# Performance work log

Measured on AMD Instinct MI355X. Metric: run time of the kernel, lower is better.

## Reference

```python
import jax, jax.numpy as jnp
import numpy as np

N, D, E, T, R, KMEM, DE = 50000, 128, 800000, 400000, 1, 32, 16
EPS = 1e-5
BETA_MAX = 5.0
GRAD_CLIP = 1.0
STATE_CLIP = 10.0
STEP = 0.1
DAMP = 0.9999  # update_damping=1.0 clamped to 1-1e-4 as in __init__


def segment_logsumexp(s, idx, n):
    # numerically-stable per-segment logsumexp; empty segments contribute 0
    m = jax.ops.segment_max(s, idx, num_segments=n)
    ms = jnp.where(jnp.isfinite(m), m, 0.0)
    z = jax.ops.segment_sum(jnp.exp(s - ms[idx]), idx, num_segments=n)
    return jnp.where(z > 0, jnp.log(jnp.maximum(z, 1e-30)) + ms, 0.0)


def setup_inputs() -> dict:
    key = jax.random.key(0)
    ks = jax.random.split(key, 24)
    inv1 = jnp.log(jnp.expm1(jnp.float32(1.0)))  # _inv_softplus(1.0)
    xav = 0.5 * np.sqrt(2.0 / (2 * D))  # xavier_uniform gain=0.5 ~ std
    inp = {
        'X': jax.random.normal(ks[0], (N, D), jnp.float32),
        'edge_attr': jax.random.normal(ks[1], (E, DE), jnp.float32),
        'ln_gamma': jnp.ones((D,), jnp.float32),
        'ln_beta': jnp.zeros((D,), jnp.float32),
        'W_Q2': jax.random.normal(ks[2], (D, D), jnp.float32) * xav,
        'W_K2': jax.random.normal(ks[3], (D, D), jnp.float32) * xav,
        'W_Q3': jax.random.normal(ks[4], (D, R * D), jnp.float32) * xav,
        'W_K3': jax.random.normal(ks[5], (D, R * D), jnp.float32) * xav,
        'T_tau': jax.random.normal(ks[6], (2, R, D), jnp.float32) * 0.02,
        'W_Qm': jax.random.normal(ks[7], (D, D), jnp.float32) * xav,
        'W_Km': jax.random.normal(ks[8], (D, D), jnp.float32) * xav,
        'B_mem': jax.random.normal(ks[9], (KMEM, D), jnp.float32) / np.sqrt(D),
        'We1': jax.random.normal(ks[10], (DE, D), jnp.float32) / np.sqrt(DE),
        'be1': jnp.zeros((D,), jnp.float32),
        'We2': jax.random.normal(ks[11], (D, 1), jnp.float32) / np.sqrt(D),
        'be2': jnp.zeros((1,), jnp.float32),
        'lambda_2': inv1, 'lambda_3': inv1, 'lambda_m': inv1,
        'beta_2': inv1, 'beta_3': inv1, 'beta_m': inv1,
        'c_2': jax.random.randint(ks[12], (E,), 0, N),
        'u_2': jax.random.randint(ks[13], (E,), 0, N),
        'c_3': jax.random.randint(ks[14], (T,), 0, N),
        'u_3': jax.random.randint(ks[15], (T,), 0, N),
        'v_3': jax.random.randint(ks[16], (T,), 0, N),
        't_tau': jax.random.randint(ks[17], (T,), 0, 2),
    }
    return inp


def reference(X, edge_attr, ln_gamma, ln_beta, W_Q2, W_K2, W_Q3, W_K3, T_tau,
              W_Qm, W_Km, B_mem, We1, be1, We2, be2,
              lambda_2, lambda_3, lambda_m, beta_2, beta_3, beta_m,
              c_2, u_2, c_3, u_3, v_3, t_tau):
    sqrt_d = jnp.sqrt(jnp.float32(D))

    def energy(Xv):
        mu = jnp.mean(Xv, axis=-1, keepdims=True)
        var = jnp.var(Xv, axis=-1, keepdims=True)
        G = (Xv - mu) * jax.lax.rsqrt(var + EPS) * ln_gamma + ln_beta
        # pairwise (order-2) energy over edge list
        b2 = jnp.minimum(jax.nn.softplus(beta_2), BETA_MAX)
        Q2, K2 = G @ W_Q2, G @ W_K2
        a2 = (jax.nn.gelu(edge_attr @ We1 + be1) @ We2 + be2)[:, 0]  # edge_mlp bias
        s2 = b2 * (jnp.sum(Q2[c_2] * K2[u_2], axis=-1) / sqrt_d) + a2  # [E]
        E2 = -(jax.nn.softplus(lambda_2) / b2) * jnp.sum(segment_logsumexp(s2, c_2, N))
        # triplet (order-3) energy with per-type tensor T_tau
        b3 = jnp.minimum(jax.nn.softplus(beta_3), BETA_MAX)
        Q3 = (G @ W_Q3).reshape(-1, R, D)
        K3 = (G @ W_K3).reshape(-1, R, D)
        s3 = b3 * jnp.einsum('erd,erd,erd,erd->e', Q3[c_3], K3[u_3], K3[v_3],
                             T_tau[t_tau]) / jnp.float32(D)  # [T]
        E3 = -(jax.nn.softplus(lambda_3) / b3) * jnp.sum(segment_logsumexp(s3, c_3, N))
        # memory-bank energy
        bm = jnp.minimum(jax.nn.softplus(beta_m), BETA_MAX)
        sm = bm * ((G @ W_Qm) @ (B_mem @ W_Km).T) / sqrt_d  # [N,K]
        Em = -(jax.nn.softplus(lambda_m) / bm) * jnp.sum(jax.nn.logsumexp(sm, axis=1))
        return E2 + E3 + Em

    Eval, gX = jax.value_and_grad(energy)(X)
    gn = jnp.maximum(jnp.linalg.norm(gX, axis=-1, keepdims=True), 1e-6)
    gX = gX * jnp.minimum(GRAD_CLIP / gn, 1.0)
    X_next = X - STEP * DAMP * gX
    sn = jnp.maximum(jnp.linalg.norm(X_next, axis=-1, keepdims=True), 1e-6)
    X_next = X_next * jnp.minimum(STATE_CLIP / sn, 1.0)
    return (X_next, Eval)
```

## Files before the change

### kernel.cpp

```cpp
#include <hip/hip_runtime.h>

#define NN 50000
#define DD 128
#define EE 800000
#define TT 400000
#define KM 32
#define UU 320
#define ROWB 12500
#define MB 782
#define EDGE_BLKS 3125
#define HB2 391
#define HBT 196
#define WCB 320
#define ZCB 196
#define FWD_TOT 11532
#define SCAN_TILE 2048
#define SCAN_NB ((NN + SCAN_TILE - 1) / SCAN_TILE)

static constexpr float INV_SQRT_D = 0.08838834764831845f;
static constexpr float INV_D = 1.f / 128.f;

typedef __attribute__((ext_vector_type(8))) short bf16x8;
typedef __attribute__((ext_vector_type(4))) float f32x4;
typedef unsigned short ushort_t;

__device__ __forceinline__ float softplus_f(float x) {
  return (x > 20.f) ? x : log1pf(__expf(x));
}

__device__ __forceinline__ float gelu_fast(float x) {
  float p = fmaf(0.044715f * x * x, x, x);
  float e = __expf(-1.5957691216057308f * p);
  return x * __builtin_amdgcn_rcpf(1.f + e);
}

__device__ __forceinline__ float wredsum(float v) {
#pragma unroll
  for (int m = 32; m; m >>= 1) v += __shfl_xor(v, m, 64);
  return v;
}

__device__ __forceinline__ float redsum16(float v) {
#pragma unroll
  for (int m = 1; m < 16; m <<= 1) v += __shfl_xor(v, m, 64);
  return v;
}

__device__ __forceinline__ float blo(unsigned w) { return __uint_as_float(w << 16); }
__device__ __forceinline__ float bhi(unsigned w) { return __uint_as_float(w & 0xffff0000u); }
__device__ __forceinline__ unsigned pack_bf16(float a, float b) {
  unsigned ua = __float_as_uint(a); ua += 0x7fff + ((ua >> 16) & 1);
  unsigned ub = __float_as_uint(b); ub += 0x7fff + ((ub >> 16) & 1);
  return (ua >> 16) | (ub & 0xffff0000u);
}
__device__ __forceinline__ ushort_t bf16_1(float x) {
  unsigned u = __float_as_uint(x); u += 0x7fff + ((u >> 16) & 1);
  return (ushort_t)(u >> 16);
}
__device__ __forceinline__ void unp8(uint4 w, float* f) {
  f[0] = blo(w.x); f[1] = bhi(w.x); f[2] = blo(w.y); f[3] = bhi(w.y);
  f[4] = blo(w.z); f[5] = bhi(w.z); f[6] = blo(w.w); f[7] = bhi(w.w);
}
__device__ __forceinline__ uint4 pk8(const float* f) {
  uint4 r;
  r.x = pack_bf16(f[0], f[1]); r.y = pack_bf16(f[2], f[3]);
  r.z = pack_bf16(f[4], f[5]); r.w = pack_bf16(f[6], f[7]);
  return r;
}

__device__ void ln_fwd_body(int bx, const float* __restrict__ X,
                            const float* __restrict__ gamma,
                            const float* __restrict__ beta,
                            unsigned* __restrict__ Gb,
                            float* __restrict__ meanv,
                            float* __restrict__ rstdv) {
  int row = bx * 4 + (threadIdx.x >> 6);
  if (row >= NN) return;
  int l = threadIdx.x & 63;
  float2 x2 = *(const float2*)(X + row * DD + 2 * l);
  float mu = wredsum(x2.x + x2.y) * (1.f / DD);
  float d0 = x2.x - mu, d1 = x2.y - mu;
  float var = wredsum(d0 * d0 + d1 * d1) * (1.f / DD);
  float rstd = rsqrtf(var + 1e-5f);
  float2 g2 = *(const float2*)(gamma + 2 * l);
  float2 b2 = *(const float2*)(beta + 2 * l);
  float o0 = d0 * rstd * g2.x + b2.x;
  float o1 = d1 * rstd * g2.y + b2.y;
  Gb[(size_t)row * 64 + l] = pack_bf16(o0, o1);
  if (l == 0) { meanv[row] = mu; rstdv[row] = rstd; }
}

__device__ void w_conv_body(int b, const float* W0, const float* W1, const float* W2,
                            const float* W3, const float* W4,
                            ushort_t* __restrict__ Wt,
                            ushort_t* __restrict__ Wc) {
  int idx = b * 256 + threadIdx.x;
  const float* Ws[5] = {W0, W1, W2, W3, W4};
  int n = idx >> 7, k = idx & 127;
  Wt[idx] = bf16_1(Ws[n >> 7][(size_t)k * 128 + (n & 127)]);
  int k2 = idx >> 7, n2 = idx & 127;
  Wc[(size_t)n2 * 640 + k2] = bf16_1(Ws[k2 >> 7][(size_t)n2 * 128 + (k2 & 127)]);
}

__device__ void gemm_km_lean(const float* __restrict__ A,
                             const float* __restrict__ W,
                             float* __restrict__ C) {
  __shared__ float As[32][129];
  int tid = threadIdx.x;
  for (int idx = tid; idx < 32 * 128; idx += 256) As[idx >> 7][idx & 127] = A[idx];
  __syncthreads();
  int r = tid >> 3, c0 = (tid & 7) * 16;
  float acc[16];
#pragma unroll
  for (int q = 0; q < 16; q++) acc[q] = 0.f;
  for (int k = 0; k < 128; k++) {
    float av = As[r][k];
#pragma unroll
    for (int q = 0; q < 16; q++) acc[q] = fmaf(av, W[k * 128 + c0 + q], acc[q]);
  }
#pragma unroll
  for (int q = 0; q < 16; q++) C[r * 128 + c0 + q] = acc[q];
}

__global__ __launch_bounds__(256) void prep_k(const float* __restrict__ X,
                                              const float* __restrict__ ln_g,
                                              const float* __restrict__ ln_b,
                                              unsigned* __restrict__ Gb,
                                              float* __restrict__ meanv,
                                              float* __restrict__ rstdv,
                                              const float* W0, const float* W1,
                                              const float* W2, const float* W3,
                                              const float* W4,
                                              ushort_t* __restrict__ Wt,
                                              ushort_t* __restrict__ Wc,
                                              const float* __restrict__ Bm,
                                              const float* __restrict__ Wkm,
                                              float* __restrict__ Km,
                                              const float* l2, const float* l3,
                                              const float* lm, const float* b2,
                                              const float* b3, const float* bm,
                                              float* __restrict__ P,
                                              float* __restrict__ eout,
                                              int* __restrict__ cnt) {
  int bx = blockIdx.x, tid = threadIdx.x;
  if (bx < ROWB) {
    ln_fwd_body(bx, X, ln_g, ln_b, Gb, meanv, rstdv);
  } else if (bx < ROWB + WCB) {
    w_conv_body(bx - ROWB, W0, W1, W2, W3, W4, Wt, Wc);
  } else if (bx == ROWB + WCB) {
    gemm_km_lean(Bm, Wkm, Km);
  } else if (bx == ROWB + WCB + 1) {
    if (tid == 0) {
      float B2 = fminf(softplus_f(b2[0]), 5.f);
      float B3 = fminf(softplus_f(b3[0]), 5.f);
      float Bm_ = fminf(softplus_f(bm[0]), 5.f);
      float S2 = softplus_f(l2[0]);
      float S3 = softplus_f(l3[0]);
      float Sm = softplus_f(lm[0]);
      P[0] = B2; P[1] = B3; P[2] = Bm_;
      P[3] = -S2 * INV_SQRT_D; P[4] = -S3 * INV_D; P[5] = -Sm * INV_SQRT_D;
      P[6] = -S2 / B2; P[7] = -S3 / B3; P[8] = -Sm / Bm_;
    }
    if (tid == 1) eout[0] = 0.f;
  } else {
    int i = (bx - (ROWB + WCB + 2)) * 1024 + tid * 4;
    if (i + 3 < 4 * NN) {
      *(int4*)&cnt[i] = (int4){0, 0, 0, 0};
    } else {
#pragma unroll
      for (int t = 0; t < 4; t++) if (i + t < 4 * NN) cnt[i + t] = 0;
    }
  }
}

__device__ void mfma_fwd_body(int bxr, int by, const ushort_t* __restrict__ Gb,
                              const ushort_t* __restrict__ Wt,
                              ushort_t* __restrict__ QK, int M, char* smem) {
  ushort_t (*sB)[136] = (ushort_t (*)[136])smem;
  int tid = threadIdx.x;
  int nb = by * 64;
  for (int idx = tid; idx < 64 * 16; idx += 256) {
    int r = idx >> 4, c8 = idx & 15;
    *(bf16x8*)&sB[r][c8 * 8] = *(const bf16x8*)(Wt + (size_t)(nb + r) * 128 + c8 * 8);
  }
  __syncthreads();
  int w = tid >> 6, l = tid & 63, quad = l >> 4, j = l & 15;
  int row0 = bxr * 64 + w * 16;
  int arow = row0 + j; if (arow >= M) arow = M - 1;
  const bf16x8* ap = (const bf16x8*)(Gb + (size_t)arow * 128);
  f32x4 acc[4];
#pragma unroll
  for (int nt = 0; nt < 4; nt++) acc[nt] = (f32x4){0.f, 0.f, 0.f, 0.f};
#pragma unroll
  for (int kc = 0; kc < 4; kc++) {
    bf16x8 a = ap[kc * 4 + quad];
#pragma unroll
    for (int nt = 0; nt < 4; nt++) {
      bf16x8 b = *(const bf16x8*)&sB[nt * 16 + j][kc * 32 + quad * 8];
      acc[nt] = __builtin_amdgcn_mfma_f32_16x16x32_bf16(a, b, acc[nt], 0, 0, 0);
    }
  }
#pragma unroll
  for (int nt = 0; nt < 4; nt++)
#pragma unroll
    for (int r = 0; r < 4; r++) {
      int row = row0 + quad * 4 + r;
      if (row < M) QK[(size_t)row * 640 + nb + nt * 16 + j] = bf16_1(acc[nt][r]);
    }
}

__device__ void edge_mlp_body(int bx, const float* __restrict__ EA,
                              const float* __restrict__ We1,
                              const float* __restrict__ be1,
                              const float* __restrict__ We2,
                              const float* __restrict__ be2,
                              float* __restrict__ a2, char* smem) {
  float* sW1 = (float*)smem;
  float* sb1 = sW1 + 2048;
  float* sW2 = sb1 + 128;
  int tid = threadIdx.x;
  for (int i = tid; i < 2048; i += 256) sW1[i] = We1[i];
  if (tid < 128) { sb1[tid] = be1[tid]; sW2[tid] = We2[tid]; }
  __syncthreads();
  int w = tid >> 6, l = tid & 63;
  int m = l & 15, q = l >> 4;
  union u8 { bf16x8 v; ushort_t s[8]; };
  u8 bf[8];
  float bb[8], ww[8];
#pragma unroll
  for (int nt = 0; nt < 8; nt++) {
    int n = nt * 16 + m;
#pragma unroll
    for (int j = 0; j < 8; j++) {
      int k = q * 8 + j;
      bf[nt].s[j] = (k < 16) ? bf16_1(sW1[k * 128 + n]) : (ushort_t)0;
    }
    bb[nt] = sb1[n];
    ww[nt] = sW2[n];
  }
  float be2v = be2[0];
  for (int batch = 0; batch < 4; batch++) {
    int e0 = bx * 256 + batch * 64 + w * 16;
    u8 af;
    if (q < 2) {
      const float* ep = EA + (size_t)(e0 + m) * 16 + q * 8;
      float4 v0 = *(const float4*)ep;
      float4 v1 = *(const float4*)(ep + 4);
      af.s[0] = bf16_1(v0.x); af.s[1] = bf16_1(v0.y);
      af.s[2] = bf16_1(v0.z); af.s[3] = bf16_1(v0.w);
      af.s[4] = bf16_1(v1.x); af.s[5] = bf16_1(v1.y);
      af.s[6] = bf16_1(v1.z); af.s[7] = bf16_1(v1.w);
    } else {
#pragma unroll
      for (int j = 0; j < 8; j++) af.s[j] = 0;
    }
    float s0 = 0.f, s1 = 0.f, s2 = 0.f, s3 = 0.f;
#pragma unroll
    for (int nt = 0; nt < 8; nt++) {
      float bias = bb[nt];
      f32x4 cin = (f32x4){bias, bias, bias, bias};
      f32x4 acc = __builtin_amdgcn_mfma_f32_16x16x32_bf16(af.v, bf[nt].v, cin, 0, 0, 0);
      float w2v = ww[nt];
      s0 = fmaf(gelu_fast(acc[0]), w2v, s0);
      s1 = fmaf(gelu_fast(acc[1]), w2v, s1);
      s2 = fmaf(gelu_fast(acc[2]), w2v, s2);
      s3 = fmaf(gelu_fast(acc[3]), w2v, s3);
    }
    s0 = redsum16(s0); s1 = redsum16(s1); s2 = redsum16(s2); s3 = redsum16(s3);
    if (m == 0) {
      int eb = e0 + q * 4;
      a2[eb + 0] = s0 + be2v;
      a2[eb + 1] = s1 + be2v;
      a2[eb + 2] = s2 + be2v;
      a2[eb + 3] = s3 + be2v;
    }
  }
}

__device__ void hist2_body(int bx, const int* __restrict__ a,
                           const int* __restrict__ b,
                           int* __restrict__ ca, int* __restrict__ cb,
                           int* __restrict__ pos_a, int* __restrict__ pos_b, int n) {
  int base = bx * 2048 + threadIdx.x;
  if (base + 1792 < n) {
    int av[8], bv[8], pa[8], pb[8];
#pragma unroll
    for (int k = 0; k < 8; k++) { int e = base + k * 256; av[k] = a[e]; bv[k] = b[e]; }
#pragma unroll
    for (int k = 0; k < 8; k++) pa[k] = atomicAdd(&ca[av[k]], 1);
#pragma unroll
    for (int k = 0; k < 8; k++) pb[k] = atomicAdd(&cb[bv[k]], 1);
#pragma unroll
    for (int k = 0; k < 8; k++) pos_a[base + k * 256] = pa[k];
#pragma unroll
    for (int k = 0; k < 8; k++) pos_b[base + k * 256] = pb[k];
  } else {
#pragma unroll
    for (int k = 0; k < 8; k++) {
      int e = base + k * 256;
      if (e < n) {
        pos_a[e] = atomicAdd(&ca[a[e]], 1);
        pos_b[e] = atomicAdd(&cb[b[e]], 1);
      }
    }
  }
}

__device__ void hist_t3_body(int bx, const int* __restrict__ c,
                             const int* __restrict__ u,
                             const int* __restrict__ v,
                             int* __restrict__ cc, int* __restrict__ cuv,
                             int* __restrict__ pos_c, int* __restrict__ pos_u,
                             int* __restrict__ pos_v, int n) {
  int base = bx * 2048 + threadIdx.x;
  if (base + 1792 < n) {
    int cv[8], uv[8], vv[8], pc[8], pu[8], pv[8];
#pragma unroll
    for (int k = 0; k < 8; k++) { int t = base + k * 256; cv[k] = c[t]; uv[k] = u[t]; vv[k] = v[t]; }
#pragma unroll
    for (int k = 0; k < 8; k++) pc[k] = atomicAdd(&cc[cv[k]], 1);
#pragma unroll
    for (int k = 0; k < 8; k++) pu[k] = atomicAdd(&cuv[uv[k]], 1);
#pragma unroll
    for (int k = 0; k < 8; k++) pv[k] = atomicAdd(&cuv[vv[k]], 1);
#pragma unroll
    for (int k = 0; k < 8; k++) pos_c[base + k * 256] = pc[k];
#pragma unroll
    for (int k = 0; k < 8; k++) pos_u[base + k * 256] = pu[k];
#pragma unroll
    for (int k = 0; k < 8; k++) pos_v[base + k * 256] = pv[k];
  } else {
#pragma unroll
    for (int k = 0; k < 8; k++) {
      int t = base + k * 256;
      if (t < n) {
        pos_c[t] = atomicAdd(&cc[c[t]], 1);
        pos_u[t] = atomicAdd(&cuv[u[t]], 1);
        pos_v[t] = atomicAdd(&cuv[v[t]], 1);
      }
    }
  }
}

__global__ __launch_bounds__(256) void fwd_k(const ushort_t* __restrict__ Gb,
                                             const ushort_t* __restrict__ Wt,
                                             ushort_t* __restrict__ QK,
                                             const float* __restrict__ EA,
                                             const float* __restrict__ We1,
                                             const float* __restrict__ be1,
                                             const float* __restrict__ We2,
                                             const float* __restrict__ be2,
                                             float* __restrict__ a2,
                                             const int* __restrict__ c2,
                                             const int* __restrict__ u2,
                                             const int* __restrict__ c3,
                                             const int* __restrict__ u3,
                                             const int* __restrict__ v3,
                                             int* __restrict__ cnt_c2,
                                             int* __restrict__ cnt_u2,
                                             int* __restrict__ cnt_c3,
                                             int* __restrict__ cnt_uv,
                                             int* __restrict__ pos_c2,
                                             int* __restrict__ pos_u2,
                                             int* __restrict__ pos_c3,
                                             int* __restrict__ pos_u3,
                                             int* __restrict__ pos_v3) {
  __shared__ char smem[64 * 136 * 2];
  int bx = (int)(((unsigned long long)blockIdx.x * 7919ull) % (unsigned long long)FWD_TOT);
  if (bx < HB2) {
    hist2_body(bx, c2, u2, cnt_c2, cnt_u2, pos_c2, pos_u2, EE);
  } else if (bx < HB2 + HBT) {
    hist_t3_body(bx - HB2, c3, u3, v3, cnt_c3, cnt_uv, pos_c3, pos_u3, pos_v3, TT);
  } else if (bx < HB2 + HBT + MB * 10) {
    int b = bx - HB2 - HBT;
    mfma_fwd_body(b / 10, b % 10, Gb, Wt, QK, NN, smem);
  } else {
    edge_mlp_body(bx - HB2 - HBT - MB * 10, EA, We1, be1, We2, be2, a2, smem);
  }
}

__global__ __launch_bounds__(256) void mfma_bwd(const ushort_t* __restrict__ dAll,
                                                const ushort_t* __restrict__ Wc,
                                                unsigned* __restrict__ dG, int M) {
  __shared__ ushort_t sB[64][40];
  int tid = threadIdx.x;
  int nb = blockIdx.y * 64;
  int w = tid >> 6, l = tid & 63, quad = l >> 4, j = l & 15;
  int row0 = blockIdx.x * 64 + w * 16;
  int arow = row0 + j; if (arow >= M) arow = M - 1;
  const ushort_t* arp = dAll + (size_t)arow * 640;
  f32x4 acc[4];
#pragma unroll
  for (int nt = 0; nt < 4; nt++) acc[nt] = (f32x4){0.f, 0.f, 0.f, 0.f};
  int sr = tid >> 2, sc = tid & 3;
  for (int kc = 0; kc < 20; kc++) {
    __syncthreads();
    *(bf16x8*)&sB[sr][sc * 8] = *(const bf16x8*)(Wc + (size_t)(nb + sr) * 640 + kc * 32 + sc * 8);
    __syncthreads();
    bf16x8 a = *(const bf16x8*)(arp + kc * 32 + quad * 8);
#pragma unroll
    for (int nt = 0; nt < 4; nt++) {
      bf16x8 b = *(const bf16x8*)&sB[nt * 16 + j][quad * 8];
      acc[nt] = __builtin_amdgcn_mfma_f32_16x16x32_bf16(a, b, acc[nt], 0, 0, 0);
    }
  }
#pragma unroll
  for (int nt = 0; nt < 4; nt++)
#pragma unroll
    for (int r = 0; r < 4; r++) {
      int row = row0 + quad * 4 + r;
      if (row < M) ((ushort_t*)dG)[(size_t)row * 128 + nb + nt * 16 + j] = bf16_1(acc[nt][r]);
    }
}

__global__ __launch_bounds__(256) void scan_p1(const int* __restrict__ cnt,
                                               int* __restrict__ part) {
  int arr = blockIdx.y, b = blockIdx.x;
  const int* c = cnt + (size_t)arr * NN;
  int gi = b * SCAN_TILE + threadIdx.x * 8;
  int s = 0;
#pragma unroll
  for (int t = 0; t < 8; t++) s += (gi + t < NN) ? c[gi + t] : 0;
#pragma unroll
  for (int m = 32; m; m >>= 1) s += __shfl_xor(s, m, 64);
  __shared__ int wt[4];
  int lane = threadIdx.x & 63, wid = threadIdx.x >> 6;
  if (lane == 0) wt[wid] = s;
  __syncthreads();
  if (threadIdx.x == 0) part[arr * SCAN_NB + b] = wt[0] + wt[1] + wt[2] + wt[3];
}

__global__ __launch_bounds__(256) void scan_p2(int* __restrict__ part) {
  int w = threadIdx.x >> 6, l = threadIdx.x & 63;
  int v = (l < SCAN_NB) ? part[w * SCAN_NB + l] : 0;
  int x = v;
#pragma unroll
  for (int d = 1; d < 64; d <<= 1) {
    int y = __shfl_up(x, d, 64);
    if (l >= d) x += y;
  }
  if (l < SCAN_NB) part[w * SCAN_NB + l] = x - v;
}

__global__ __launch_bounds__(256) void scan_p3(const int* __restrict__ cnt,
                                               const int* __restrict__ part,
                                               int* __restrict__ rowptr) {
  int arr = blockIdx.y, b = blockIdx.x;
  const int* c = cnt + (size_t)arr * NN;
  int* rp = rowptr + (size_t)arr * (NN + 1);
  int tid = threadIdx.x;
  int gi = b * SCAN_TILE + tid * 8;
  int vals[8];
#pragma unroll
  for (int t = 0; t < 8; t++) vals[t] = (gi + t < NN) ? c[gi + t] : 0;
  int tsum = 0;
#pragma unroll
  for (int t = 0; t < 8; t++) tsum += vals[t];
  int lane = tid & 63, wid = tid >> 6;
  int x = tsum;
#pragma unroll
  for (int d = 1; d < 64; d <<= 1) {
    int y = __shfl_up(x, d, 64);
    if (lane >= d) x += y;
  }
  __shared__ int wt[4];
  if (lane == 63) wt[wid] = x;
  __syncthreads();
  int wadd = 0;
  for (int w = 0; w < wid; w++) wadd += wt[w];
  int running = part[arr * SCAN_NB + b] + wadd + x - tsum;
#pragma unroll
  for (int t = 0; t < 8; t++) {
    if (gi + t < NN) rp[gi + t] = running;
    running += vals[t];
  }
  if (b == SCAN_NB - 1 && tid == 255) rp[NN] = running;
}

__device__ void scat2_body(int bx, const int* __restrict__ c2,
                           const int* __restrict__ u2,
                           const float* __restrict__ a2,
                           const int* __restrict__ posc,
                           const int* __restrict__ posu,
                           const int* __restrict__ rpc,
                           const int* __restrict__ rpu,
                           uint2* __restrict__ payc,
                           uint2* __restrict__ payu, int n) {
  int base = bx * 2048 + threadIdx.x;
  if (base + 1792 < n) {
    int c[8], u[8]; float a[8]; int pc[8], pu[8];
#pragma unroll
    for (int k = 0; k < 8; k++) {
      int e = base + k * 256;
      c[k] = c2[e]; u[k] = u2[e]; a[k] = a2[e]; pc[k] = posc[e]; pu[k] = posu[e];
    }
    int p[8], q[8];
#pragma unroll
    for (int k = 0; k < 8; k++) { p[k] = rpc[c[k]] + pc[k]; q[k] = rpu[u[k]] + pu[k]; }
#pragma unroll
    for (int k = 0; k < 8; k++) {
      uint2 t; t.x = (unsigned)u[k]; t.y = __float_as_uint(a[k]);
      payc[p[k]] = t;
    }
#pragma unroll
    for (int k = 0; k < 8; k++) {
      uint2 t; t.x = (unsigned)p[k]; t.y = (unsigned)c[k];
      payu[q[k]] = t;
    }
  } else {
#pragma unroll
    for (int k = 0; k < 8; k++) {
      int e = base + k * 256;
      if (e < n) {
        int cc = c2[e], uu = u2[e];
        int pp = rpc[cc] + posc[e];
        int qq = rpu[uu] + posu[e];
        uint2 t; t.x = (unsigned)uu; t.y = __float_as_uint(a2[e]);
        payc[pp] = t;
        uint2 t2; t2.x = (unsigned)pp; t2.y = (unsigned)cc;
        payu[qq] = t2;
      }
    }
  }
}

__device__ void scat_t3_body(int bx, const int* __restrict__ c3,
                             const int* __restrict__ u3,
                             const int* __restrict__ v3,
                             const int* __restrict__ ttau,
                             const int* __restrict__ posc,
                             const int* __restrict__ posu,
                             const int* __restrict__ posv,
                             const int* __restrict__ rpc,
                             const int* __restrict__ rpuv,
                             uint2* __restrict__ payc,
                             uint2* __restrict__ payuv, int n) {
  int base = bx * 2048 + threadIdx.x;
  if (base + 1792 < n) {
    int c[8], u[8], v[8], ta[8], p[8], q1[8], q2[8];
#pragma unroll
    for (int k = 0; k < 8; k++) {
      int t = base + k * 256;
      c[k] = c3[t]; u[k] = u3[t]; v[k] = v3[t]; ta[k] = ttau[t] & 1;
    }
#pragma unroll
    for (int k = 0; k < 8; k++) {
      int t = base + k * 256;
      p[k] = rpc[c[k]] + posc[t];
      q1[k] = rpuv[u[k]] + posu[t];
      q2[k] = rpuv[v[k]] + posv[t];
    }
#pragma unroll
    for (int k = 0; k < 8; k++) {
      uint2 a; a.x = ((unsigned)u[k] << 16) | (unsigned)v[k]; a.y = (unsigned)ta[k];
      payc[p[k]] = a;
    }
#pragma unroll
    for (int k = 0; k < 8; k++) {
      unsigned sp = ((unsigned)p[k] << 1) | (unsigned)ta[k];
      uint2 b1; b1.x = ((unsigned)v[k] << 16) | (unsigned)c[k]; b1.y = sp;
      payuv[q1[k]] = b1;
      uint2 b2; b2.x = ((unsigned)u[k] << 16) | (unsigned)c[k]; b2.y = sp;
      payuv[q2[k]] = b2;
    }
  } else {
#pragma unroll
    for (int k = 0; k < 8; k++) {
      int t = base + k * 256;
      if (t < n) {
        int c = c3[t], u = u3[t], v = v3[t], ta = ttau[t] & 1;
        int p = rpc[c] + posc[t];
        int q1 = rpuv[u] + posu[t];
        int q2 = rpuv[v] + posv[t];
        unsigned sp = ((unsigned)p << 1) | (unsigned)ta;
        uint2 a; a.x = ((unsigned)u << 16) | (unsigned)v; a.y = (unsigned)ta;
        payc[p] = a;
        uint2 b1; b1.x = ((unsigned)v << 16) | (unsigned)c; b1.y = sp;
        payuv[q1] = b1;
        uint2 b2; b2.x = ((unsigned)u << 16) | (unsigned)c; b2.y = sp;
        payuv[q2] = b2;
      }
    }
  }
}

__global__ __launch_bounds__(256) void scat_k(const int* __restrict__ c2,
                                              const int* __restrict__ u2,
                                              const float* __restrict__ a2,
                                              const int* __restrict__ pos_c2,
                                              const int* __restrict__ pos_u2,
                                              const int* __restrict__ rp_c2,
                                              const int* __restrict__ rp_u2,
                                              uint2* __restrict__ payc2,
                                              uint2* __restrict__ payu2,
                                              const int* __restrict__ c3,
                                              const int* __restrict__ u3,
                                              const int* __restrict__ v3,
                                              const int* __restrict__ ttau,
                                              const int* __restrict__ pos_c3,
                                              const int* __restrict__ pos_u3,
                                              const int* __restrict__ pos_v3,
                                              const int* __restrict__ rp_c3,
                                              const int* __restrict__ rp_uv,
                                              uint2* __restrict__ payc3,
                                              uint2* __restrict__ payuv) {
  int b3 = blockIdx.x / 3, r = blockIdx.x % 3;
  if (r < 2) {
    int b = b3 * 2 + r;
    if (b < HB2) scat2_body(b, c2, u2, a2, pos_c2, pos_u2, rp_c2, rp_u2, payc2, payu2, EE);
  } else {
    scat_t3_body(b3, c3, u3, v3, ttau, pos_c3, pos_u3, pos_v3,
                 rp_c3, rp_uv, payc3, payuv, TT);
  }
}

__device__ void e2_body(int bx, const unsigned* __restrict__ QK,
                        const float* __restrict__ P,
                        const uint2* __restrict__ pay,
                        const int* __restrict__ rp,
                        float* __restrict__ s2c,
                        float* __restrict__ L2,
                        unsigned* __restrict__ dAll) {
  int row = bx * 4 + (threadIdx.x >> 6);
  int l = threadIdx.x & 63, g = l >> 4, j = l & 15;
  float b2s = P[0] * INV_SQRT_D, cw2 = P[3];
  float q[8];
  unp8(*(const uint4*)(QK + (size_t)row * UU + j * 4), q);
  int s = rp[row], e = rp[row + 1];
  float m = -3.0e38f, z = 0.f;
  float acc[8] = {0.f, 0.f, 0.f, 0.f, 0.f, 0.f, 0.f, 0.f};
  int i0 = s + g;
  uint4 kA1 = {0,0,0,0}, kA2 = {0,0,0,0}, kB1 = {0,0,0,0}, kB2 = {0,0,0,0};
  float aA1 = 0.f, aA2 = 0.f, aB1 = 0.f, aB2 = 0.f;
  if (i0 < e)      { uint2 w = pay[i0];      aA1 = __uint_as_float(w.y); kA1 = *(const uint4*)(QK + (size_t)w.x * UU + 64 + j * 4); }
  if (i0 + 4 < e)  { uint2 w = pay[i0 + 4];  aA2 = __uint_as_float(w.y); kA2 = *(const uint4*)(QK + (size_t)w.x * UU + 64 + j * 4); }
  if (i0 + 8 < e)  { uint2 w = pay[i0 + 8];  aB1 = __uint_as_float(w.y); kB1 = *(const uint4*)(QK + (size_t)w.x * UU + 64 + j * 4); }
  if (i0 + 12 < e) { uint2 w = pay[i0 + 12]; aB2 = __uint_as_float(w.y); kB2 = *(const uint4*)(QK + (size_t)w.x * UU + 64 + j * 4); }
  for (int i = i0; i < e; i += 8) {
    uint4 kC1 = {0,0,0,0}, kC2 = {0,0,0,0}; float aC1 = 0.f, aC2 = 0.f;
    if (i + 16 < e) { uint2 w = pay[i + 16]; aC1 = __uint_as_float(w.y); kC1 = *(const uint4*)(QK + (size_t)w.x * UU + 64 + j * 4); }
    if (i + 20 < e) { uint2 w = pay[i + 20]; aC2 = __uint_as_float(w.y); kC2 = *(const uint4*)(QK + (size_t)w.x * UU + 64 + j * 4); }
    {
      float k[8]; unp8(kA1, k);
      float d = 0.f;
#pragma unroll
      for (int t = 0; t < 8; t++) d = fmaf(q[t], k[t], d);
      d = redsum16(d);
      float sv = b2s * d + aA1;
      if (j == 0) s2c[i] = sv;
      if (sv <= m) {
        float p = __expf(sv - m);
        z += p;
#pragma unroll
        for (int t = 0; t < 8; t++) acc[t] = fmaf(p, k[t], acc[t]);
      } else {
        float r = __expf(m - sv);
        z = fmaf(z, r, 1.f);
#pragma unroll
        for (int t = 0; t < 8; t++) acc[t] = fmaf(acc[t], r, k[t]);
        m = sv;
      }
    }
    if (i + 4 < e) {
      float k[8]; unp8(kA2, k);
      float d = 0.f;
#pragma unroll
      for (int t = 0; t < 8; t++) d = fmaf(q[t], k[t], d);
      d = redsum16(d);
      float sv = b2s * d + aA2;
      if (j == 0) s2c[i + 4] = sv;
      if (sv <= m) {
        float p = __expf(sv - m);
        z += p;
#pragma unroll
        for (int t = 0; t < 8; t++) acc[t] = fmaf(p, k[t], acc[t]);
      } else {
        float r = __expf(m - sv);
        z = fmaf(z, r, 1.f);
#pragma unroll
        for (int t = 0; t < 8; t++) acc[t] = fmaf(acc[t], r, k[t]);
        m = sv;
      }
    }
    kA1 = kB1; aA1 = aB1; kA2 = kB2; aA2 = aB2;
    kB1 = kC1; aB1 = aC1; kB2 = kC2; aB2 = aC2;
  }
  float mx = fmaxf(m, __shfl_xor(m, 16, 64));
  mx = fmaxf(mx, __shfl_xor(mx, 32, 64));
  float r = (z > 0.f) ? __expf(m - mx) : 0.f;
  float zz = z * r;
  zz += __shfl_xor(zz, 16, 64);
  zz += __shfl_xor(zz, 32, 64);
#pragma unroll
  for (int t = 0; t < 8; t++) {
    float v = acc[t] * r;
    v += __shfl_xor(v, 16, 64);
    v += __shfl_xor(v, 32, 64);
    acc[t] = v;
  }
  if (l == 0) L2[row] = (zz > 0.f) ? (mx + __logf(zz)) : 0.f;
  if (g == 0) {
    float coef = (zz > 0.f) ? cw2 / zz : 0.f;
    float o[8];
#pragma unroll
    for (int t = 0; t < 8; t++) o[t] = coef * acc[t];
    *(uint4*)(dAll + (size_t)row * UU + 0 + j * 4) = pk8(o);
  }
}

__device__ void t3_body(int bx, const unsigned* __restrict__ QK,
                        const float* __restrict__ P,
                        const uint2* __restrict__ pay,
                        const int* __restrict__ rp,
                        float* __restrict__ s3c,
                        float* __restrict__ L3,
// ... 129 lines not shown
}

__global__ __launch_bounds__(256) void phase2_k(const unsigned* __restrict__ QK,
                                                const float* __restrict__ Tt,
                                                const float* __restrict__ Km,
                                                const float* __restrict__ P,
                                                const uint2* __restrict__ payc2,
                                                const int* __restrict__ rp_c2,
                                                const uint2* __restrict__ payc3,
                                                const int* __restrict__ rp_c3,
                                                float* __restrict__ s2c,
                                                float* __restrict__ L2,
                                                float* __restrict__ s3c,
                                                float* __restrict__ L3,
                                                float* __restrict__ Lm,
                                                unsigned* __restrict__ dAll) {
  __shared__ float smem[32 * 144];
  int bx = blockIdx.x;
  int body = bx % 3, b = bx / 3;
  int tid = threadIdx.x;
  if (body == 0) {
    e2_body(b, QK, P, payc2, rp_c2, s2c, L2, dAll);
  } else if (body == 1) {
    {
      int ta = tid >> 7, d = tid & 127;
      smem[ta * 144 + (d >> 3) * 9 + (d & 7)] = Tt[tid];
    }
    __syncthreads();
    t3_body(b, QK, P, payc3, rp_c3, s3c, L3, dAll, smem);
  } else {
    for (int i = tid; i < KM * DD; i += 256) {
      int k = i >> 7, d = i & 127;
      smem[k * 144 + (d >> 3) * 9 + (d & 7)] = Km[i];
    }
    __syncthreads();
    em_body(b, QK, P, dAll, Lm, smem);
  }
}

__device__ void dk2_body(int bx, const unsigned* __restrict__ QK,
                         const float* __restrict__ s2c,
                         const float* __restrict__ L2,
                         const float* __restrict__ P,
                         const uint2* __restrict__ pay,
                         const int* __restrict__ rp,
                         unsigned* __restrict__ dAll) {
  int row = bx * 4 + (threadIdx.x >> 6);
  int l = threadIdx.x & 63, g = l >> 4, j = l & 15;
  float cw2 = P[3];
  int s = rp[row], e = rp[row + 1];
  float acc[8] = {0.f, 0.f, 0.f, 0.f, 0.f, 0.f, 0.f, 0.f};
  int i0 = s + g;
  uint4 qA1 = {0,0,0,0}, qA2 = {0,0,0,0}, qB1 = {0,0,0,0}, qB2 = {0,0,0,0};
  float scA1 = 0.f, lcA1 = 0.f, scA2 = 0.f, lcA2 = 0.f;
  float scB1 = 0.f, lcB1 = 0.f, scB2 = 0.f, lcB2 = 0.f;
  if (i0 < e)      { uint2 w = pay[i0];      scA1 = s2c[w.x]; lcA1 = L2[w.y]; qA1 = *(const uint4*)(QK + (size_t)w.y * UU + 0 + j * 4); }
  if (i0 + 4 < e)  { uint2 w = pay[i0 + 4];  scA2 = s2c[w.x]; lcA2 = L2[w.y]; qA2 = *(const uint4*)(QK + (size_t)w.y * UU + 0 + j * 4); }
  if (i0 + 8 < e)  { uint2 w = pay[i0 + 8];  scB1 = s2c[w.x]; lcB1 = L2[w.y]; qB1 = *(const uint4*)(QK + (size_t)w.y * UU + 0 + j * 4); }
  if (i0 + 12 < e) { uint2 w = pay[i0 + 12]; scB2 = s2c[w.x]; lcB2 = L2[w.y]; qB2 = *(const uint4*)(QK + (size_t)w.y * UU + 0 + j * 4); }
  for (int i = i0; i < e; i += 8) {
    uint4 qC1 = {0,0,0,0}, qC2 = {0,0,0,0};
    float scC1 = 0.f, lcC1 = 0.f, scC2 = 0.f, lcC2 = 0.f;
    if (i + 16 < e) { uint2 w = pay[i + 16]; scC1 = s2c[w.x]; lcC1 = L2[w.y]; qC1 = *(const uint4*)(QK + (size_t)w.y * UU + 0 + j * 4); }
    if (i + 20 < e) { uint2 w = pay[i + 20]; scC2 = s2c[w.x]; lcC2 = L2[w.y]; qC2 = *(const uint4*)(QK + (size_t)w.y * UU + 0 + j * 4); }
    {
      float w1 = cw2 * __expf(scA1 - lcA1);
      float qv[8]; unp8(qA1, qv);
#pragma unroll
      for (int t = 0; t < 8; t++) acc[t] = fmaf(w1, qv[t], acc[t]);
    }
    if (i + 4 < e) {
      float w2 = cw2 * __expf(scA2 - lcA2);
      float qv[8]; unp8(qA2, qv);
#pragma unroll
      for (int t = 0; t < 8; t++) acc[t] = fmaf(w2, qv[t], acc[t]);
    }
    qA1 = qB1; scA1 = scB1; lcA1 = lcB1; qA2 = qB2; scA2 = scB2; lcA2 = lcB2;
    qB1 = qC1; scB1 = scC1; lcB1 = lcC1; qB2 = qC2; scB2 = scC2; lcB2 = lcC2;
  }
#pragma unroll
  for (int t = 0; t < 8; t++) {
    float v = acc[t];
    v += __shfl_xor(v, 16, 64);
    v += __shfl_xor(v, 32, 64);
    acc[t] = v;
  }
  if (g == 0) *(uint4*)(dAll + (size_t)row * UU + 64 + j * 4) = pk8(acc);
}

__device__ void dk3_body(int bx, const unsigned* __restrict__ QK,
                         const float* __restrict__ s3c,
                         const float* __restrict__ L3,
                         const float* __restrict__ P,
                         const uint2* __restrict__ pay,
                         const int* __restrict__ rp,
                         unsigned* __restrict__ dAll,
                         const float* __restrict__ sT) {
  int tid = threadIdx.x;
  int row = bx * 4 + (tid >> 6);
  int l = tid & 63, g = l >> 4, j = l & 15;
  float cw3 = P[4];
  int s = rp[row], e = rp[row + 1];
  float acc[8] = {0.f, 0.f, 0.f, 0.f, 0.f, 0.f, 0.f, 0.f};
  int i0 = s + g;
  uint4 qA = {0,0,0,0}, kA = {0,0,0,0};
  uint4 qB = {0,0,0,0}, kB = {0,0,0,0};
  int taA = 0, taB = 0;
  float scA = 0.f, lcA = 0.f, scB = 0.f, lcB = 0.f;
  if (i0 < e) {
    uint2 w = pay[i0]; int o = w.x >> 16, c = w.x & 0xffff; unsigned sp = w.y;
    taA = (int)(sp & 1); scA = s3c[sp >> 1]; lcA = L3[c];
    qA = *(const uint4*)(QK + (size_t)c * UU + 128 + j * 4);
    kA = *(const uint4*)(QK + (size_t)o * UU + 192 + j * 4);
  }
  if (i0 + 4 < e) {
    uint2 w = pay[i0 + 4]; int o = w.x >> 16, c = w.x & 0xffff; unsigned sp = w.y;
    taB = (int)(sp & 1); scB = s3c[sp >> 1]; lcB = L3[c];
    qB = *(const uint4*)(QK + (size_t)c * UU + 128 + j * 4);
    kB = *(const uint4*)(QK + (size_t)o * UU + 192 + j * 4);
  }
  for (int i = i0; i < e; i += 4) {
    uint4 qC = {0,0,0,0}, kC = {0,0,0,0}; int taC = 0;
    float scC = 0.f, lcC = 0.f;
    if (i + 8 < e) {
      uint2 w = pay[i + 8]; int o = w.x >> 16, c = w.x & 0xffff; unsigned sp = w.y;
      taC = (int)(sp & 1); scC = s3c[sp >> 1]; lcC = L3[c];
      qC = *(const uint4*)(QK + (size_t)c * UU + 128 + j * 4);
      kC = *(const uint4*)(QK + (size_t)o * UU + 192 + j * 4);
    }
    float w = cw3 * __expf(scA - lcA);
    float qv[8], ko[8]; unp8(qA, qv); unp8(kA, ko);
    const float* tv = &sT[taA * 144 + j * 9];
#pragma unroll
    for (int t = 0; t < 8; t++) acc[t] = fmaf(w * tv[t], qv[t] * ko[t], acc[t]);
    qA = qB; kA = kB; taA = taB; scA = scB; lcA = lcB;
    qB = qC; kB = kC; taB = taC; scB = scC; lcB = lcC;
  }
#pragma unroll
  for (int t = 0; t < 8; t++) {
    float v = acc[t];
    v += __shfl_xor(v, 16, 64);
    v += __shfl_xor(v, 32, 64);
    acc[t] = v;
  }
  if (g == 0) *(uint4*)(dAll + (size_t)row * UU + 192 + j * 4) = pk8(acc);
}

__device__ void eval_write_body(int bx, const float* __restrict__ L2,
                                const float* __restrict__ L3,
                                const float* __restrict__ Lm,
                                const float* __restrict__ P,
                                float* __restrict__ out) {
  int i = bx * 256 + threadIdx.x;
  float a2 = 0.f, a3 = 0.f, am = 0.f;
  if (i < NN) { a2 = L2[i]; a3 = L3[i]; am = Lm[i]; }
  a2 = wredsum(a2); a3 = wredsum(a3); am = wredsum(am);
  __shared__ float r2[4], r3[4], rm[4];
  int wv = threadIdx.x >> 6, l = threadIdx.x & 63;
  if (l == 0) { r2[wv] = a2; r3[wv] = a3; rm[wv] = am; }
  __syncthreads();
  if (threadIdx.x == 0) {
    float S2 = r2[0] + r2[1] + r2[2] + r2[3];
    float S3 = r3[0] + r3[1] + r3[2] + r3[3];
    float Sm = rm[0] + rm[1] + rm[2] + rm[3];
    atomicAdd(out, P[6] * S2 + P[7] * S3 + P[8] * Sm);
  }
}

__global__ __launch_bounds__(256) void phase3_k(const unsigned* __restrict__ QK,
                                                const float* __restrict__ Tt,
                                                const float* __restrict__ P,
                                                const float* __restrict__ s2c,
                                                const float* __restrict__ L2,
                                                const uint2* __restrict__ payu2,
                                                const int* __restrict__ rp_u2,
                                                const float* __restrict__ s3c,
                                                const float* __restrict__ L3,
                                                const uint2* __restrict__ payuv,
                                                const int* __restrict__ rp_uv,
                                                unsigned* __restrict__ dAll,
                                                const float* __restrict__ Lm,
                                                float* __restrict__ eout) {
  __shared__ float smem[2 * 144];
  int bx = blockIdx.x;
  int tid = threadIdx.x;
  if (bx < 2 * ROWB) {
    int body = bx & 1, b = bx >> 1;
    if (body == 0) {
      dk2_body(b, QK, s2c, L2, P, payu2, rp_u2, dAll);
    } else {
      {
        int ta = tid >> 7, d = tid & 127;
        smem[ta * 144 + (d >> 3) * 9 + (d & 7)] = Tt[tid];
      }
      __syncthreads();
      dk3_body(b, QK, s3c, L3, P, payuv, rp_uv, dAll, smem);
    }
  } else {
    eval_write_body(bx - 2 * ROWB, L2, L3, Lm, P, eout);
  }
}

__global__ __launch_bounds__(256) void fin_k(const float* __restrict__ X,
                                             const unsigned* __restrict__ dG,
                                             const float* __restrict__ gamma,
                                             const float* __restrict__ meanv,
                                             const float* __restrict__ rstdv,
                                             float* __restrict__ out) {
  int row = blockIdx.x * 4 + (threadIdx.x >> 6);
  if (row >= NN) return;
  int l = threadIdx.x & 63;
  float mu = meanv[row], rstd = rstdv[row];
  float2 x2 = *(const float2*)(X + row * DD + 2 * l);
  unsigned gw = dG[(size_t)row * 64 + l];
  float2 ga = *(const float2*)(gamma + 2 * l);
  float xh0 = (x2.x - mu) * rstd, xh1 = (x2.y - mu) * rstd;
  float dh0 = blo(gw) * ga.x, dh1 = bhi(gw) * ga.y;
  float sa = wredsum(dh0 + dh1) * (1.f / DD);
  float sb = wredsum(dh0 * xh0 + dh1 * xh1) * (1.f / DD);
  float dx0 = rstd * (dh0 - sa - xh0 * sb);
  float dx1 = rstd * (dh1 - sa - xh1 * sb);
  float gn = fmaxf(sqrtf(wredsum(dx0 * dx0 + dx1 * dx1)), 1e-6f);
  float sc = fminf(1.f / gn, 1.f);
  dx0 *= sc; dx1 *= sc;
  float xn0 = x2.x - 0.1f * 0.9999f * dx0;
  float xn1 = x2.y - 0.1f * 0.9999f * dx1;
  float sn = fmaxf(sqrtf(wredsum(xn0 * xn0 + xn1 * xn1)), 1e-6f);
  float sc2 = fminf(10.f / sn, 1.f);
  float2 o; o.x = xn0 * sc2; o.y = xn1 * sc2;
  *(float2*)(out + row * DD + 2 * l) = o;
}

extern "C" void kernel_launch(void* const* d_in, const int* in_sizes, int n_in,
                              void* d_out, int out_size, void* d_ws, size_t ws_size,
                              hipStream_t stream) {
  (void)in_sizes; (void)n_in; (void)out_size;
  const float* X = (const float*)d_in[0];
  const float* EA = (const float*)d_in[1];
  const float* ln_g = (const float*)d_in[2];
  const float* ln_b = (const float*)d_in[3];
  const float* W_Q2 = (const float*)d_in[4];
  const float* W_K2 = (const float*)d_in[5];
  const float* W_Q3 = (const float*)d_in[6];
  const float* W_K3 = (const float*)d_in[7];
  const float* T_tau = (const float*)d_in[8];
  const float* W_Qm = (const float*)d_in[9];
  const float* W_Km = (const float*)d_in[10];
  const float* B_mem = (const float*)d_in[11];
  const float* We1 = (const float*)d_in[12];
  const float* be1 = (const float*)d_in[13];
  const float* We2 = (const float*)d_in[14];
  const float* be2 = (const float*)d_in[15];
  const float* l2s = (const float*)d_in[16];
  const float* l3s = (const float*)d_in[17];
  const float* lms = (const float*)d_in[18];
  const float* b2s = (const float*)d_in[19];
  const float* b3s = (const float*)d_in[20];
  const float* bms = (const float*)d_in[21];
  const int* c2 = (const int*)d_in[22];
  const int* u2 = (const int*)d_in[23];
  const int* c3 = (const int*)d_in[24];
  const int* u3 = (const int*)d_in[25];
  const int* v3 = (const int*)d_in[26];
  const int* ttau = (const int*)d_in[27];
  float* out = (float*)d_out;

  float* ws = (float*)d_ws;
  size_t off = 0;
  auto alloc = [&](size_t n) { float* p = ws + off; off += n; return p; };
  const size_t ND = (size_t)NN * DD;
  unsigned* Gb = (unsigned*)alloc(ND / 2);
  unsigned* QKall = (unsigned*)alloc((size_t)NN * UU);
  unsigned* dAll = (unsigned*)alloc((size_t)NN * UU);
  unsigned* dG = (unsigned*)alloc(ND / 2);
  ushort_t* Wt5 = (ushort_t*)alloc(640 * 128 / 2);
  ushort_t* Wcat = (ushort_t*)alloc(640 * 128 / 2);
  float* Km = alloc((size_t)KM * DD);
  float* a2 = alloc(EE);
  float* s2c = alloc(EE);
  float* s3c = alloc(TT);
  float* meanv = alloc(NN);
  float* rstdv = alloc(NN);
  float* L2 = alloc(NN);
  float* L3 = alloc(NN);
  float* Lm = alloc(NN);
  float* Pparams = alloc(16);
  int* cnt = (int*)alloc(4 * (size_t)NN);
  int* rowptr = (int*)alloc(4 * (size_t)(NN + 1));
  int* spart = (int*)alloc(4 * SCAN_NB);
  int* pos_c2 = (int*)alloc(EE);
  int* pos_u2 = (int*)alloc(EE);
  int* pos_c3 = (int*)alloc(TT);
  int* pos_u3 = (int*)alloc(TT);
  int* pos_v3 = (int*)alloc(TT);
  uint2* payc2 = (uint2*)alloc(2 * (size_t)EE);
  uint2* payu2 = (uint2*)alloc(2 * (size_t)EE);
  uint2* payc3 = (uint2*)alloc(2 * (size_t)TT);
  uint2* payuv = (uint2*)alloc(4 * (size_t)TT);
  if (off * sizeof(float) > ws_size) return;

  int* cnt_c2 = cnt, *cnt_u2 = cnt + NN, *cnt_c3 = cnt + 2 * NN, *cnt_uv = cnt + 3 * NN;
  int* rp_c2 = rowptr, *rp_u2 = rowptr + (NN + 1), *rp_c3 = rowptr + 2 * (NN + 1), *rp_uv = rowptr + 3 * (NN + 1);

  prep_k<<<ROWB + WCB + 2 + ZCB, 256, 0, stream>>>(
      X, ln_g, ln_b, Gb, meanv, rstdv,
      W_Q2, W_K2, W_Q3, W_K3, W_Qm, Wt5, Wcat,
      B_mem, W_Km, Km,
      l2s, l3s, lms, b2s, b3s, bms, Pparams, out + ND, cnt);

  fwd_k<<<FWD_TOT, 256, 0, stream>>>(
      (const ushort_t*)Gb, Wt5, (ushort_t*)QKall,
      EA, We1, be1, We2, be2, a2,
      c2, u2, c3, u3, v3,
      cnt_c2, cnt_u2, cnt_c3, cnt_uv,
      pos_c2, pos_u2, pos_c3, pos_u3, pos_v3);

  scan_p1<<<dim3(SCAN_NB, 4), 256, 0, stream>>>(cnt, spart);
  scan_p2<<<1, 256, 0, stream>>>(spart);
  scan_p3<<<dim3(SCAN_NB, 4), 256, 0, stream>>>(cnt, spart, rowptr);

  scat_k<<<3 * HBT, 256, 0, stream>>>(
      c2, u2, a2, pos_c2, pos_u2, rp_c2, rp_u2, payc2, payu2,
      c3, u3, v3, ttau, pos_c3, pos_u3, pos_v3, rp_c3, rp_uv, payc3, payuv);

  phase2_k<<<3 * ROWB, 256, 0, stream>>>(QKall, T_tau, Km, Pparams,
                                         payc2, rp_c2, payc3, rp_c3,
                                         s2c, L2, s3c, L3, Lm, dAll);
  phase3_k<<<2 * ROWB + 196, 256, 0, stream>>>(QKall, T_tau, Pparams,
                                               s2c, L2, payu2, rp_u2,
                                               s3c, L3, payuv, rp_uv, dAll,
                                               Lm, out + ND);

  mfma_bwd<<<dim3(MB, 2), 256, 0, stream>>>((const ushort_t*)dAll, Wcat, dG, NN);

  fin_k<<<ROWB, 256, 0, stream>>>(X, dG, ln_g, meanv, rstdv, out);
}
```

Before: 723.3 us.

## Move histogram atomics to prep kernel and stage GEMM outputs through LDS

The atomic histogram and position blocks move from the forward GEMM kernel into the prep kernel. The count zeroing that prep_k used to do becomes a hipMemsetAsync placed before it. The forward and backward MFMA GEMMs now write their bf16 output tiles to shared memory first and then store them as 16-byte vectors per row, replacing the scattered 2-byte stores. This is meant to coalesce output writes and rebalance work between the two kernels. It adds an extra memset launch and an LDS round-trip.

```diff
diff --git a/kernel.cpp b/kernel.cpp
--- a/kernel.cpp
+++ b/kernel.cpp
@@ -11,9 +11,9 @@
 #define EDGE_BLKS 3125
 #define HB2 391
 #define HBT 196
+#define HIST_TOT 587
 #define WCB 320
-#define ZCB 196
-#define FWD_TOT 11532
+#define FWD_TOT 10945
 #define SCAN_TILE 2048
 #define SCAN_NB ((NN + SCAN_TILE - 1) / SCAN_TILE)
 
@@ -66,6 +66,71 @@
   r.x = pack_bf16(f[0], f[1]); r.y = pack_bf16(f[2], f[3]);
   r.z = pack_bf16(f[4], f[5]); r.w = pack_bf16(f[6], f[7]);
   return r;
+}
+
+__device__ void hist2_body(int bx, const int* __restrict__ a,
+                           const int* __restrict__ b,
+                           int* __restrict__ ca, int* __restrict__ cb,
+                           int* __restrict__ pos_a, int* __restrict__ pos_b, int n) {
+  int base = bx * 2048 + threadIdx.x;
+  if (base + 1792 < n) {
+    int av[8], bv[8], pa[8], pb[8];
+#pragma unroll
+    for (int k = 0; k < 8; k++) { int e = base + k * 256; av[k] = a[e]; bv[k] = b[e]; }
+#pragma unroll
+    for (int k = 0; k < 8; k++) pa[k] = atomicAdd(&ca[av[k]], 1);
+#pragma unroll
+    for (int k = 0; k < 8; k++) pb[k] = atomicAdd(&cb[bv[k]], 1);
+#pragma unroll
+    for (int k = 0; k < 8; k++) pos_a[base + k * 256] = pa[k];
+#pragma unroll
+    for (int k = 0; k < 8; k++) pos_b[base + k * 256] = pb[k];
+  } else {
+#pragma unroll
+    for (int k = 0; k < 8; k++) {
+      int e = base + k * 256;
+      if (e < n) {
+        pos_a[e] = atomicAdd(&ca[a[e]], 1);
+        pos_b[e] = atomicAdd(&cb[b[e]], 1);
+      }
+    }
+  }
+}
+
+__device__ void hist_t3_body(int bx, const int* __restrict__ c,
+                             const int* __restrict__ u,
+                             const int* __restrict__ v,
+                             int* __restrict__ cc, int* __restrict__ cuv,
+                             int* __restrict__ pos_c, int* __restrict__ pos_u,
+                             int* __restrict__ pos_v, int n) {
+  int base = bx * 2048 + threadIdx.x;
+  if (base + 1792 < n) {
+    int cv[8], uv[8], vv[8], pc[8], pu[8], pv[8];
+#pragma unroll
+    for (int k = 0; k < 8; k++) { int t = base + k * 256; cv[k] = c[t]; uv[k] = u[t]; vv[k] = v[t]; }
+#pragma unroll
+    for (int k = 0; k < 8; k++) pc[k] = atomicAdd(&cc[cv[k]], 1);
+#pragma unroll
+    for (int k = 0; k < 8; k++) pu[k] = atomicAdd(&cuv[uv[k]], 1);
+#pragma unroll
+    for (int k = 0; k < 8; k++) pv[k] = atomicAdd(&cuv[vv[k]], 1);
+#pragma unroll
+    for (int k = 0; k < 8; k++) pos_c[base + k * 256] = pc[k];
+#pragma unroll
+    for (int k = 0; k < 8; k++) pos_u[base + k * 256] = pu[k];
+#pragma unroll
+    for (int k = 0; k < 8; k++) pos_v[base + k * 256] = pv[k];
+  } else {
+#pragma unroll
+    for (int k = 0; k < 8; k++) {
+      int t = base + k * 256;
+      if (t < n) {
+        pos_c[t] = atomicAdd(&cc[c[t]], 1);
+        pos_u[t] = atomicAdd(&cuv[u[t]], 1);
+        pos_v[t] = atomicAdd(&cuv[v[t]], 1);
+      }
+    }
+  }
 }
 
 __device__ void ln_fwd_body(int bx, const float* __restrict__ X,
@@ -141,15 +206,32 @@
                                               const float* b3, const float* bm,
                                               float* __restrict__ P,
                                               float* __restrict__ eout,
-                                              int* __restrict__ cnt) {
+                                              const int* __restrict__ c2,
+                                              const int* __restrict__ u2,
+                                              const int* __restrict__ c3,
+                                              const int* __restrict__ u3,
+                                              const int* __restrict__ v3,
+                                              int* __restrict__ cnt_c2,
+                                              int* __restrict__ cnt_u2,
+                                              int* __restrict__ cnt_c3,
+                                              int* __restrict__ cnt_uv,
+                                              int* __restrict__ pos_c2,
+                                              int* __restrict__ pos_u2,
+                                              int* __restrict__ pos_c3,
+                                              int* __restrict__ pos_u3,
+                                              int* __restrict__ pos_v3) {
   int bx = blockIdx.x, tid = threadIdx.x;
-  if (bx < ROWB) {
-    ln_fwd_body(bx, X, ln_g, ln_b, Gb, meanv, rstdv);
-  } else if (bx < ROWB + WCB) {
-    w_conv_body(bx - ROWB, W0, W1, W2, W3, W4, Wt, Wc);
-  } else if (bx == ROWB + WCB) {
+  if (bx < HB2) {
+    hist2_body(bx, c2, u2, cnt_c2, cnt_u2, pos_c2, pos_u2, EE);
+  } else if (bx < HIST_TOT) {
+    hist_t3_body(bx - HB2, c3, u3, v3, cnt_c3, cnt_uv, pos_c3, pos_u3, pos_v3, TT);
+  } else if (bx < HIST_TOT + ROWB) {
+    ln_fwd_body(bx - HIST_TOT, X, ln_g, ln_b, Gb, meanv, rstdv);
+  } else if (bx < HIST_TOT + ROWB + WCB) {
+    w_conv_body(bx - HIST_TOT - ROWB, W0, W1, W2, W3, W4, Wt, Wc);
+  } else if (bx == HIST_TOT + ROWB + WCB) {
     gemm_km_lean(Bm, Wkm, Km);
-  } else if (bx == ROWB + WCB + 1) {
+  } else {
     if (tid == 0) {
       float B2 = fminf(softplus_f(b2[0]), 5.f);
       float B3 = fminf(softplus_f(b3[0]), 5.f);
@@ -162,14 +244,6 @@
       P[6] = -S2 / B2; P[7] = -S3 / B3; P[8] = -Sm / Bm_;
     }
     if (tid == 1) eout[0] = 0.f;
-  } else {
-    int i = (bx - (ROWB + WCB + 2)) * 1024 + tid * 4;
-    if (i + 3 < 4 * NN) {
-      *(int4*)&cnt[i] = (int4){0, 0, 0, 0};
-    } else {
-#pragma unroll
-      for (int t = 0; t < 4; t++) if (i + t < 4 * NN) cnt[i + t] = 0;
-    }
   }
 }
 
@@ -200,13 +274,22 @@
       acc[nt] = __builtin_amdgcn_mfma_f32_16x16x32_bf16(a, b, acc[nt], 0, 0, 0);
     }
   }
+  __syncthreads();
+  ushort_t* sC = (ushort_t*)smem + w * 1184;
 #pragma unroll
   for (int nt = 0; nt < 4; nt++)
 #pragma unroll
-    for (int r = 0; r < 4; r++) {
-      int row = row0 + quad * 4 + r;
-      if (row < M) QK[(size_t)row * 640 + nb + nt * 16 + j] = bf16_1(acc[nt][r]);
-    }
+    for (int r = 0; r < 4; r++)
+      sC[(quad * 4 + r) * 72 + nt * 16 + j] = bf16_1(acc[nt][r]);
+  int rr = l >> 3, cc = l & 7;
+#pragma unroll
+  for (int it = 0; it < 2; it++) {
+    int row = row0 + it * 8 + rr;
+    if (row < M) {
+      uint4 val = *(const uint4*)&sC[(it * 8 + rr) * 72 + cc * 8];
+      *(uint4*)(QK + (size_t)row * 640 + nb + cc * 8) = val;
+    }
+  }
 }
 
 __device__ void edge_mlp_body(int bx, const float* __restrict__ EA,
@@ -277,71 +360,6 @@
   }
 }
 
-__device__ void hist2_body(int bx, const int* __restrict__ a,
-                           const int* __restrict__ b,
-                           int* __restrict__ ca, int* __restrict__ cb,
-                           int* __restrict__ pos_a, int* __restrict__ pos_b, int n) {
-  int base = bx * 2048 + threadIdx.x;
-  if (base + 1792 < n) {
-    int av[8], bv[8], pa[8], pb[8];
-#pragma unroll
-    for (int k = 0; k < 8; k++) { int e = base + k * 256; av[k] = a[e]; bv[k] = b[e]; }
-#pragma unroll
-    for (int k = 0; k < 8; k++) pa[k] = atomicAdd(&ca[av[k]], 1);
-#pragma unroll
-    for (int k = 0; k < 8; k++) pb[k] = atomicAdd(&cb[bv[k]], 1);
-#pragma unroll
-    for (int k = 0; k < 8; k++) pos_a[base + k * 256] = pa[k];
-#pragma unroll
-    for (int k = 0; k < 8; k++) pos_b[base + k * 256] = pb[k];
-  } else {
-#pragma unroll
-    for (int k = 0; k < 8; k++) {
-      int e = base + k * 256;
-      if (e < n) {
-        pos_a[e] = atomicAdd(&ca[a[e]], 1);
-        pos_b[e] = atomicAdd(&cb[b[e]], 1);
-      }
-    }
-  }
-}
-
-__device__ void hist_t3_body(int bx, const int* __restrict__ c,
-                             const int* __restrict__ u,
-                             const int* __restrict__ v,
-                             int* __restrict__ cc, int* __restrict__ cuv,
-                             int* __restrict__ pos_c, int* __restrict__ pos_u,
-                             int* __restrict__ pos_v, int n) {
-  int base = bx * 2048 + threadIdx.x;
-  if (base + 1792 < n) {
-    int cv[8], uv[8], vv[8], pc[8], pu[8], pv[8];
-#pragma unroll
-    for (int k = 0; k < 8; k++) { int t = base + k * 256; cv[k] = c[t]; uv[k] = u[t]; vv[k] = v[t]; }
-#pragma unroll
-    for (int k = 0; k < 8; k++) pc[k] = atomicAdd(&cc[cv[k]], 1);
-#pragma unroll
-    for (int k = 0; k < 8; k++) pu[k] = atomicAdd(&cuv[uv[k]], 1);
-#pragma unroll
-    for (int k = 0; k < 8; k++) pv[k] = atomicAdd(&cuv[vv[k]], 1);
-#pragma unroll
-    for (int k = 0; k < 8; k++) pos_c[base + k * 256] = pc[k];
-#pragma unroll
-    for (int k = 0; k < 8; k++) pos_u[base + k * 256] = pu[k];
-#pragma unroll
-    for (int k = 0; k < 8; k++) pos_v[base + k * 256] = pv[k];
-  } else {
-#pragma unroll
-    for (int k = 0; k < 8; k++) {
-      int t = base + k * 256;
-      if (t < n) {
-        pos_c[t] = atomicAdd(&cc[c[t]], 1);
-        pos_u[t] = atomicAdd(&cuv[u[t]], 1);
-        pos_v[t] = atomicAdd(&cuv[v[t]], 1);
-      }
-    }
-  }
-}
-
 __global__ __launch_bounds__(256) void fwd_k(const ushort_t* __restrict__ Gb,
                                              const ushort_t* __restrict__ Wt,
                                              ushort_t* __restrict__ QK,
@@ -350,39 +368,21 @@
                                              const float* __restrict__ be1,
                                              const float* __restrict__ We2,
                                              const float* __restrict__ be2,
-                                             float* __restrict__ a2,
-                                             const int* __restrict__ c2,
-                                             const int* __restrict__ u2,
-                                             const int* __restrict__ c3,
-                                             const int* __restrict__ u3,
-                                             const int* __restrict__ v3,
-                                             int* __restrict__ cnt_c2,
-                                             int* __restrict__ cnt_u2,
-                                             int* __restrict__ cnt_c3,
-                                             int* __restrict__ cnt_uv,
-                                             int* __restrict__ pos_c2,
-                                             int* __restrict__ pos_u2,
-                                             int* __restrict__ pos_c3,
-                                             int* __restrict__ pos_u3,
-                                             int* __restrict__ pos_v3) {
+                                             float* __restrict__ a2) {
   __shared__ char smem[64 * 136 * 2];
   int bx = (int)(((unsigned long long)blockIdx.x * 7919ull) % (unsigned long long)FWD_TOT);
-  if (bx < HB2) {
-    hist2_body(bx, c2, u2, cnt_c2, cnt_u2, pos_c2, pos_u2, EE);
-  } else if (bx < HB2 + HBT) {
-    hist_t3_body(bx - HB2, c3, u3, v3, cnt_c3, cnt_uv, pos_c3, pos_u3, pos_v3, TT);
-  } else if (bx < HB2 + HBT + MB * 10) {
-    int b = bx - HB2 - HBT;
-    mfma_fwd_body(b / 10, b % 10, Gb, Wt, QK, NN, smem);
+  if (bx < MB * 10) {
+    mfma_fwd_body(bx / 10, bx % 10, Gb, Wt, QK, NN, smem);
   } else {
-    edge_mlp_body(bx - HB2 - HBT - MB * 10, EA, We1, be1, We2, be2, a2, smem);
+    edge_mlp_body(bx - MB * 10, EA, We1, be1, We2, be2, a2, smem);
   }
 }
 
 __global__ __launch_bounds__(256) void mfma_bwd(const ushort_t* __restrict__ dAll,
                                                 const ushort_t* __restrict__ Wc,
                                                 unsigned* __restrict__ dG, int M) {
-  __shared__ ushort_t sB[64][40];
+  __shared__ char smem[4 * 1184 * 2];
+  ushort_t (*sB)[40] = (ushort_t (*)[40])smem;
   int tid = threadIdx.x;
   int nb = blockIdx.y * 64;
   int w = tid >> 6, l = tid & 63, quad = l >> 4, j = l & 15;
@@ -404,13 +404,23 @@
       acc[nt] = __builtin_amdgcn_mfma_f32_16x16x32_bf16(a, b, acc[nt], 0, 0, 0);
     }
   }
+  __syncthreads();
+  ushort_t* sC = (ushort_t*)smem + w * 1184;
 #pragma unroll
   for (int nt = 0; nt < 4; nt++)
 #pragma unroll
-    for (int r = 0; r < 4; r++) {
-      int row = row0 + quad * 4 + r;
-      if (row < M) ((ushort_t*)dG)[(size_t)row * 128 + nb + nt * 16 + j] = bf16_1(acc[nt][r]);
-    }
+    for (int r = 0; r < 4; r++)
+      sC[(quad * 4 + r) * 72 + nt * 16 + j] = bf16_1(acc[nt][r]);
+  int rr = l >> 3, cc = l & 7;
+  ushort_t* dGs = (ushort_t*)dG;
+#pragma unroll
+  for (int it = 0; it < 2; it++) {
+    int row = row0 + it * 8 + rr;
+    if (row < M) {
+      uint4 val = *(const uint4*)&sC[(it * 8 + rr) * 72 + cc * 8];
+      *(uint4*)(dGs + (size_t)row * 128 + nb + cc * 8) = val;
+    }
+  }
 }
 
 __global__ __launch_bounds__(256) void scan_p1(const int* __restrict__ cnt,
@@ -1146,18 +1156,20 @@
   int* cnt_c2 = cnt, *cnt_u2 = cnt + NN, *cnt_c3 = cnt + 2 * NN, *cnt_uv = cnt + 3 * NN;
   int* rp_c2 = rowptr, *rp_u2 = rowptr + (NN + 1), *rp_c3 = rowptr + 2 * (NN + 1), *rp_uv = rowptr + 3 * (NN + 1);
 
-  prep_k<<<ROWB + WCB + 2 + ZCB, 256, 0, stream>>>(
+  hipMemsetAsync(cnt, 0, 4ull * NN * sizeof(int), stream);
+
+  prep_k<<<HIST_TOT + ROWB + WCB + 2, 256, 0, stream>>>(
       X, ln_g, ln_b, Gb, meanv, rstdv,
       W_Q2, W_K2, W_Q3, W_K3, W_Qm, Wt5, Wcat,
       B_mem, W_Km, Km,
-      l2s, l3s, lms, b2s, b3s, bms, Pparams, out + ND, cnt);
-
-  fwd_k<<<FWD_TOT, 256, 0, stream>>>(
-      (const ushort_t*)Gb, Wt5, (ushort_t*)QKall,
-      EA, We1, be1, We2, be2, a2,
+      l2s, l3s, lms, b2s, b3s, bms, Pparams, out + ND,
       c2, u2, c3, u3, v3,
       cnt_c2, cnt_u2, cnt_c3, cnt_uv,
       pos_c2, pos_u2, pos_c3, pos_u3, pos_v3);
+
+  fwd_k<<<FWD_TOT, 256, 0, stream>>>(
+      (const ushort_t*)Gb, Wt5, (ushort_t*)QKall,
+      EA, We1, be1, We2, be2, a2);
 
   scan_p1<<<dim3(SCAN_NB, 4), 256, 0, stream>>>(cnt, spart);
   scan_p2<<<1, 256, 0, stream>>>(spart);
```

After: 764.6 us. 1.06x slower.
